# Optimization experiments

Measured on AMD Instinct MI355X. Metric: run time of the kernel, lower is better.

## Reference

```python
import jax, jax.numpy as jnp
import numpy as np

XI = 4.0  # init kwarg


def _gaussian_kernel(xi: float):
    radius = int(3 * xi)
    coords = jnp.arange(-radius, radius + 1, dtype=jnp.float32)
    g1 = jnp.exp(-coords ** 2 / (2 * xi * xi))
    g1 = g1 / g1.sum()
    # dense 3D outer-product kernel, shape (K, K, K)
    g3 = g1[:, None, None] * g1[None, :, None] * g1[None, None, :]
    K = g3.shape[0]
    # grouped depthwise weight: (out=3, in/groups=1, K, K, K)
    return jnp.broadcast_to(g3[None, None], (3, 1, K, K, K))


def setup_inputs() -> dict:
    key = jax.random.key(0)
    x = jax.random.normal(key, (1, 3, 160, 160, 160), dtype=jnp.float32)
    kernel = _gaussian_kernel(XI)
    return {"x": x, "kernel": kernel}


def reference(x, kernel):
    # grouped Conv3d, groups=3 (depthwise), 'same' padding of radius each side
    r = (kernel.shape[-1] - 1) // 2
    return jax.lax.conv_general_dilated(
        x, kernel,
        window_strides=(1, 1, 1),
        padding=[(r, r), (r, r), (r, r)],
        dimension_numbers=("NCDHW", "OIDHW", "NCDHW"),
        feature_group_count=3,
    )
```

## Files before the change

### kernel.cpp

```cpp
#include <hip/hip_runtime.h>
#include <hip/hip_fp16.h>


#define NV 160
constexpr int KS    = 25;
constexpr int RAD   = 12;
constexpr int PLANE = NV * NV;
constexpr int VOL   = NV * NV * NV;
constexpr int TOT   = 3 * VOL;
constexpr int ROWS  = NV + 2 * RAD;

constexpr int PITCH = 17;
constexpr int OPT   = 10;
constexpr int WIN   = OPT + KS - 1;
constexpr int OROW  = 168;

constexpr int HC2   = 80;
constexpr int TR    = HC2 + 2 * RAD;
constexpr int TP2   = 84;
constexpr int ATASK = 64 * 20;
constexpr int BTASK = 40 * 20;

__device__ __forceinline__ void pk(float2& a, float2 g, float2 v) {
    asm("v_pk_fma_f32 %0, %1, %2, %0" : "+v"(a) : "v"(g), "v"(v));
}

__device__ __forceinline__ void load_g(const float* __restrict__ k3, float* g) {
    float c   = k3[12 * 625 + 312];
    float g12 = cbrtf(c);
    float inv = 1.0f / (g12 * g12);
#pragma unroll
    for (int t = 0; t < KS; ++t) g[t] = k3[t * 625 + 312] * inv;
}

__global__ __launch_bounds__(256) void conv_w(const float* __restrict__ in,
                                              __half* __restrict__ out,
                                              const float* __restrict__ k3) {
    __shared__ float2 T[ROWS][PITCH];
    float gs[KS];
    load_g(k3, gs);
    float2 g2[KS];
#pragma unroll
    for (int t = 0; t < KS; ++t) g2[t] = make_float2(gs[t], gs[t]);

    int tid = threadIdx.x;
    int b   = blockIdx.x;
    int ht  = b % 5;
    int cd  = b / 5;
    int h0  = ht * 32;
    const float* base = in + (size_t)cd * PLANE;

    int wl = tid & 31, hq = tid >> 5;
#pragma unroll
    for (int hh = 0; hh < 2; ++hh) {
        int hp = hq + hh * 8;
        const float* r0 = base + (h0 + 2 * hp) * NV;
#pragma unroll
        for (int ib = 0; ib < ROWS; ib += 32) {
            int i = ib + wl;
            if (i < ROWS) {
                int wv = i - RAD;
                float a = 0.f, bb = 0.f;
                if (wv >= 0 && wv < NV) { a = r0[wv]; bb = r0[NV + wv]; }
                T[i][hp] = make_float2(a, bb);
            }
        }
    }
    __syncthreads();

    int p  = tid & 15;
    int ct = tid >> 4;
    int wb = ct * OPT;
    float2 acc[OPT];
#pragma unroll
    for (int j = 0; j < OPT; ++j) acc[j] = make_float2(0.f, 0.f);
#pragma unroll
    for (int it = 0; it < WIN; ++it) {
        float2 v = T[wb + it][p];
#pragma unroll
        for (int j = 0; j < OPT; ++j) {
            int t = it - j;
            if (t >= 0 && t < KS) pk(acc[j], g2[t], v);
        }
    }

    __syncthreads();
    __half* Ost = (__half*)(&T[0][0]);
#pragma unroll
    for (int j = 0; j < OPT; ++j) {
        Ost[(2 * p)     * OROW + wb + j] = __float2half_rn(acc[j].x);
        Ost[(2 * p + 1) * OROW + wb + j] = __float2half_rn(acc[j].y);
    }
    __syncthreads();
    __half* ob = out + (size_t)cd * PLANE + (size_t)h0 * NV;
#pragma unroll
    for (int it = 0; it < 3; ++it) {
        int task = it * 256 + tid;
        if (task < 640) {
            int chunk = task % 20, row = task / 20;
            uint4 v = *(const uint4*)(Ost + row * OROW + 8 * chunk);
            *(uint4*)(ob + (size_t)row * NV + 8 * chunk) = v;
        }
    }
}

__global__ __launch_bounds__(320) void conv_h(const __half* __restrict__ in,
                                              __half* __restrict__ out,
                                              const float* __restrict__ k3) {
    __shared__ __half2 T[TR][TP2];
    float gs[KS];
    load_g(k3, gs);
    float2 g2[KS];
#pragma unroll
    for (int t = 0; t < KS; ++t) g2[t] = make_float2(gs[t], gs[t]);

    int tid = threadIdx.x;
    int b   = blockIdx.x;
    int hh  = b & 1;
    int cd  = b >> 1;
    int h0  = hh * HC2;
    const __half* base = in + (size_t)cd * PLANE;

    uint4 rA[4];
#pragma unroll
    for (int i = 0; i < 4; ++i) {
        int task = i * 320 + tid;
        int r = task / 20, k = task % 20;
        int hg = h0 - RAD + r;
        rA[i] = make_uint4(0u, 0u, 0u, 0u);
        if (hg >= 0 && hg < NV) rA[i] = *(const uint4*)(base + hg * NV + 8 * k);
    }
#pragma unroll
    for (int i = 0; i < 4; ++i) {
        int task = i * 320 + tid;
        int r = task / 20, k = task % 20;
        *(uint4*)(&T[r][4 * k]) = rA[i];
    }
    uint4 rB[3];
#pragma unroll
    for (int i = 0; i < 3; ++i) {
        int task = i * 320 + tid;
        rB[i] = make_uint4(0u, 0u, 0u, 0u);
        if (task < BTASK) {
            int r = 64 + task / 20, k = task % 20;
            int hg = h0 - RAD + r;
            if (hg >= 0 && hg < NV) rB[i] = *(const uint4*)(base + hg * NV + 8 * k);
        }
    }
    asm volatile("s_waitcnt lgkmcnt(0)" ::: "memory");
    __builtin_amdgcn_s_barrier();
    __builtin_amdgcn_sched_barrier(0);

    int wp = tid % 80, oc = tid / 80;
    {
        int rb = oc * OPT;
        float2 acc[OPT];
#pragma unroll
        for (int j = 0; j < OPT; ++j) acc[j] = make_float2(0.f, 0.f);
#pragma unroll
        for (int it = 0; it < WIN; ++it) {
            float2 v = __half22float2(T[rb + it][wp]);
#pragma unroll
            for (int j = 0; j < OPT; ++j) {
                int t = it - j;
                if (t >= 0 && t < KS) pk(acc[j], g2[t], v);
            }
        }
        __half* op = out + (size_t)cd * PLANE + (size_t)(h0 + rb) * NV + 2 * wp;
#pragma unroll
        for (int j = 0; j < OPT; ++j)
            *(__half2*)(op + j * NV) = __float22half2_rn(acc[j]);
    }
    __builtin_amdgcn_sched_barrier(0);
#pragma unroll
    for (int i = 0; i < 3; ++i) {
        int task = i * 320 + tid;
        if (task < BTASK) {
            int r = 64 + task / 20, k = task % 20;
            *(uint4*)(&T[r][4 * k]) = rB[i];
        }
    }
    asm volatile("s_waitcnt lgkmcnt(0)" ::: "memory");
    __builtin_amdgcn_s_barrier();
    __builtin_amdgcn_sched_barrier(0);
    {
        int rb = (oc + 4) * OPT;
        float2 acc[OPT];
#pragma unroll
        for (int j = 0; j < OPT; ++j) acc[j] = make_float2(0.f, 0.f);
#pragma unroll
        for (int it = 0; it < WIN; ++it) {
            float2 v = __half22float2(T[rb + it][wp]);
#pragma unroll
            for (int j = 0; j < OPT; ++j) {
                int t = it - j;
                if (t >= 0 && t < KS) pk(acc[j], g2[t], v);
            }
        }
        __half* op = out + (size_t)cd * PLANE + (size_t)(h0 + rb) * NV + 2 * wp;
#pragma unroll
        for (int j = 0; j < OPT; ++j)
            *(__half2*)(op + j * NV) = __float22half2_rn(acc[j]);
    }
}

__global__ __launch_bounds__(320) void conv_d(const __half* __restrict__ in,
                                              float* __restrict__ out,
                                              const float* __restrict__ k3) {
    __shared__ __half2 T[TR][TP2];
    float gs[KS];
    load_g(k3, gs);
    float2 g2[KS];
#pragma unroll
    for (int t = 0; t < KS; ++t) g2[t] = make_float2(gs[t], gs[t]);

    int tid = threadIdx.x;
    int b   = blockIdx.x;
    int dh  = b & 1;
    int ch  = b >> 1;
    int c   = ch / NV, h = ch % NV;
    int d0  = dh * HC2;
    const __half* base = in + (size_t)c * VOL + h * NV;

    uint4 rA[4];
#pragma unroll
    for (int i = 0; i < 4; ++i) {
        int task = i * 320 + tid;
        int r = task / 20, k = task % 20;
        int dg = d0 - RAD + r;
        rA[i] = make_uint4(0u, 0u, 0u, 0u);
        if (dg >= 0 && dg < NV)
            rA[i] = *(const uint4*)(base + (size_t)dg * PLANE + 8 * k);
    }
#pragma unroll
    for (int i = 0; i < 4; ++i) {
        int task = i * 320 + tid;
        int r = task / 20, k = task % 20;
        *(uint4*)(&T[r][4 * k]) = rA[i];
    }
    uint4 rB[3];
#pragma unroll
    for (int i = 0; i < 3; ++i) {
        int task = i * 320 + tid;
        rB[i] = make_uint4(0u, 0u, 0u, 0u);
        if (task < BTASK) {
            int r = 64 + task / 20, k = task % 20;
            int dg = d0 - RAD + r;
            if (dg >= 0 && dg < NV)
                rB[i] = *(const uint4*)(base + (size_t)dg * PLANE + 8 * k);
        }
    }
    asm volatile("s_waitcnt lgkmcnt(0)" ::: "memory");
    __builtin_amdgcn_s_barrier();
    __builtin_amdgcn_sched_barrier(0);

    int wp = tid % 80, oc = tid / 80;
    {
        int rb = oc * OPT;
        float2 acc[OPT];
#pragma unroll
        for (int j = 0; j < OPT; ++j) acc[j] = make_float2(0.f, 0.f);
#pragma unroll
        for (int it = 0; it < WIN; ++it) {
            float2 v = __half22float2(T[rb + it][wp]);
#pragma unroll
            for (int j = 0; j < OPT; ++j) {
                int t = it - j;
                if (t >= 0 && t < KS) pk(acc[j], g2[t], v);
            }
        }
        float* op = out + (size_t)c * VOL + h * NV + 2 * wp;
#pragma unroll
        for (int j = 0; j < OPT; ++j)
            *(float2*)(op + (size_t)(d0 + rb + j) * PLANE) = acc[j];
    }
    __builtin_amdgcn_sched_barrier(0);
#pragma unroll
    for (int i = 0; i < 3; ++i) {
        int task = i * 320 + tid;
        if (task < BTASK) {
            int r = 64 + task / 20, k = task % 20;
            *(uint4*)(&T[r][4 * k]) = rB[i];
        }
    }
    asm volatile("s_waitcnt lgkmcnt(0)" ::: "memory");
    __builtin_amdgcn_s_barrier();
    __builtin_amdgcn_sched_barrier(0);
    {
        int rb = (oc + 4) * OPT;
        float2 acc[OPT];
#pragma unroll
        for (int j = 0; j < OPT; ++j) acc[j] = make_float2(0.f, 0.f);
#pragma unroll
        for (int it = 0; it < WIN; ++it) {
            float2 v = __half22float2(T[rb + it][wp]);
#pragma unroll
            for (int j = 0; j < OPT; ++j) {
                int t = it - j;
                if (t >= 0 && t < KS) pk(acc[j], g2[t], v);
            }
        }
        float* op = out + (size_t)c * VOL + h * NV + 2 * wp;
#pragma unroll
        for (int j = 0; j < OPT; ++j)
            *(float2*)(op + (size_t)(d0 + rb + j) * PLANE) = acc[j];
    }
}

__global__ __launch_bounds__(256) void conv3d_direct(const float* __restrict__ x,
                                                     const float* __restrict__ k3,
                                                     float* __restrict__ out) {
    int idx = blockIdx.x * 256 + threadIdx.x;
    if (idx >= TOT) return;
    int w = idx % NV;
    int t = idx / NV;
    int h = t % NV; t /= NV;
    int d = t % NV;
    int c = t / NV;
    const float* kc = k3 + c * (KS * KS * KS);
    float acc = 0.f;
    for (int i = 0; i < KS; ++i) {
        int dd = d + i - RAD;
        if (dd < 0 || dd >= NV) continue;
        for (int j = 0; j < KS; ++j) {
            int hh = h + j - RAD;
            if (hh < 0 || hh >= NV) continue;
            const float* xr = x + (c * NV + dd) * NV * NV + hh * NV + (w - RAD);
            const float* kr = kc + (i * KS + j) * KS;
            int k0 = (RAD - w) > 0 ? (RAD - w) : 0;
            int k1 = (NV + RAD - w) < KS ? (NV + RAD - w) : KS;
            for (int k = k0; k < k1; ++k) acc += kr[k] * xr[k];
        }
    }
    out[idx] = acc;
}

extern "C" void kernel_launch(void* const* d_in, const int* in_sizes, int n_in,
                              void* d_out, int out_size, void* d_ws, size_t ws_size,
                              hipStream_t stream) {
    const float* x  = (const float*)d_in[0];
    const float* k3 = (const float*)d_in[1];
    float* out = (float*)d_out;

    if (ws_size >= (size_t)TOT * 2 * sizeof(__half)) {
        __half* tmpA = (__half*)d_ws;
        __half* tmpB = tmpA + TOT;
        conv_w<<<2400, 256, 0, stream>>>(x, tmpA, k3);
        conv_h<<<480 * 2, 320, 0, stream>>>(tmpA, tmpB, k3);
        conv_d<<<480 * 2, 320, 0, stream>>>(tmpB, out, k3);
    } else {
        conv3d_direct<<<(TOT + 255) / 256, 256, 0, stream>>>(x, k3, out);
    }
}
```

Measured before the change: 61.28 us.

## Load conv_h/conv_d halo tiles directly into LDS with global_load_lds

Replaces the register-staged global-to-LDS copies in the H and D passes with direct global_load_lds DMA into an unpadded shared tile. Out-of-range halo rows are zero-filled by explicit LDS stores, and the tile base shifts per half. The second half of the tile is waited on with partial vmcnt counts, so the first compute pass overlaps the tail of the load. This removes register pressure and the VGPR round trip, but drops the padding that avoided bank conflicts and depends on exact vmcnt ordering for correctness.

```diff
diff --git a/kernel.cpp b/kernel.cpp
--- a/kernel.cpp
+++ b/kernel.cpp
@@ -15,11 +15,12 @@
 constexpr int WIN   = OPT + KS - 1;
 constexpr int OROW  = 168;
 
-constexpr int HC2   = 80;
-constexpr int TR    = HC2 + 2 * RAD;
-constexpr int TP2   = 84;
-constexpr int ATASK = 64 * 20;
-constexpr int BTASK = 40 * 20;
+constexpr int HC2    = 80;
+constexpr int TR     = 104;
+constexpr int TPW    = 80;
+constexpr int VROWS  = 92;
+constexpr int VSLOTS = VROWS * 20;
+constexpr int ZSLOTS = 12 * 20;
 
 __device__ __forceinline__ void pk(float2& a, float2 g, float2 v) {
     asm("v_pk_fma_f32 %0, %1, %2, %0" : "+v"(a) : "v"(g), "v"(v));
@@ -31,6 +32,12 @@
     float inv = 1.0f / (g12 * g12);
 #pragma unroll
     for (int t = 0; t < KS; ++t) g[t] = k3[t * 625 + 312] * inv;
+}
+
+__device__ __forceinline__ void gll16(const void* g, void* l) {
+    __builtin_amdgcn_global_load_lds(
+        (const __attribute__((address_space(1))) void*)g,
+        (__attribute__((address_space(3))) void*)l, 16, 0, 0);
 }
 
 __global__ __launch_bounds__(256) void conv_w(const float* __restrict__ in,
@@ -107,7 +114,7 @@
 __global__ __launch_bounds__(320) void conv_h(const __half* __restrict__ in,
                                               __half* __restrict__ out,
                                               const float* __restrict__ k3) {
-    __shared__ __half2 T[TR][TP2];
+    __shared__ __half2 T[TR][TPW];
     float gs[KS];
     load_g(k3, gs);
     float2 g2[KS];
@@ -119,35 +126,30 @@
     int hh  = b & 1;
     int cd  = b >> 1;
     int h0  = hh * HC2;
-    const __half* base = in + (size_t)cd * PLANE;
-
-    uint4 rA[4];
-#pragma unroll
-    for (int i = 0; i < 4; ++i) {
-        int task = i * 320 + tid;
-        int r = task / 20, k = task % 20;
-        int hg = h0 - RAD + r;
-        rA[i] = make_uint4(0u, 0u, 0u, 0u);
-        if (hg >= 0 && hg < NV) rA[i] = *(const uint4*)(base + hg * NV + 8 * k);
-    }
-#pragma unroll
-    for (int i = 0; i < 4; ++i) {
-        int task = i * 320 + tid;
-        int r = task / 20, k = task % 20;
-        *(uint4*)(&T[r][4 * k]) = rA[i];
-    }
-    uint4 rB[3];
-#pragma unroll
-    for (int i = 0; i < 3; ++i) {
-        int task = i * 320 + tid;
-        rB[i] = make_uint4(0u, 0u, 0u, 0u);
-        if (task < BTASK) {
-            int r = 64 + task / 20, k = task % 20;
-            int hg = h0 - RAD + r;
-            if (hg >= 0 && hg < NV) rB[i] = *(const uint4*)(base + hg * NV + 8 * k);
-        }
-    }
-    asm volatile("s_waitcnt lgkmcnt(0)" ::: "memory");
+    char* Tf = (char*)(&T[0][0]);
+
+    int zbase = (hh == 0) ? 0 : 92 * 320;
+    if (tid < ZSLOTS)
+        *(uint4*)(Tf + zbase + tid * 16) = make_uint4(0u, 0u, 0u, 0u);
+
+    int vbase = (hh == 0) ? 12 * 320 : 0;
+    const char* gsrc = (const char*)(in + (size_t)cd * PLANE
+                                     + (size_t)((hh == 0) ? 0 : 68) * NV);
+    int wavebase = tid & ~63;
+#pragma unroll
+    for (int it = 0; it < 4; ++it) {
+        int sw = it * 320 + wavebase;
+        gll16(gsrc + (size_t)(sw + (tid & 63)) * 16, Tf + vbase + sw * 16);
+    }
+#pragma unroll
+    for (int it = 4; it < 6; ++it) {
+        int slot = it * 320 + tid;
+        if (slot < VSLOTS) {
+            int sw = it * 320 + wavebase;
+            gll16(gsrc + (size_t)slot * 16, Tf + vbase + sw * 16);
+        }
+    }
+    asm volatile("s_waitcnt vmcnt(2) lgkmcnt(0)" ::: "memory");
     __builtin_amdgcn_s_barrier();
     __builtin_amdgcn_sched_barrier(0);
 
@@ -172,15 +174,7 @@
             *(__half2*)(op + j * NV) = __float22half2_rn(acc[j]);
     }
     __builtin_amdgcn_sched_barrier(0);
-#pragma unroll
-    for (int i = 0; i < 3; ++i) {
-        int task = i * 320 + tid;
-        if (task < BTASK) {
-            int r = 64 + task / 20, k = task % 20;
-            *(uint4*)(&T[r][4 * k]) = rB[i];
-        }
-    }
-    asm volatile("s_waitcnt lgkmcnt(0)" ::: "memory");
+    asm volatile("s_waitcnt vmcnt(0)" ::: "memory");
     __builtin_amdgcn_s_barrier();
     __builtin_amdgcn_sched_barrier(0);
     {
@@ -207,7 +201,7 @@
 __global__ __launch_bounds__(320) void conv_d(const __half* __restrict__ in,
                                               float* __restrict__ out,
                                               const float* __restrict__ k3) {
-    __shared__ __half2 T[TR][TP2];
+    __shared__ __half2 T[TR][TPW];
     float gs[KS];
     load_g(k3, gs);
     float2 g2[KS];
@@ -220,37 +214,34 @@
     int ch  = b >> 1;
     int c   = ch / NV, h = ch % NV;
     int d0  = dh * HC2;
-    const __half* base = in + (size_t)c * VOL + h * NV;
-
-    uint4 rA[4];
-#pragma unroll
-    for (int i = 0; i < 4; ++i) {
-        int task = i * 320 + tid;
-        int r = task / 20, k = task % 20;
-        int dg = d0 - RAD + r;
-        rA[i] = make_uint4(0u, 0u, 0u, 0u);
-        if (dg >= 0 && dg < NV)
-            rA[i] = *(const uint4*)(base + (size_t)dg * PLANE + 8 * k);
-    }
-#pragma unroll
-    for (int i = 0; i < 4; ++i) {
-        int task = i * 320 + tid;
-        int r = task / 20, k = task % 20;
-        *(uint4*)(&T[r][4 * k]) = rA[i];
-    }
-    uint4 rB[3];
-#pragma unroll
-    for (int i = 0; i < 3; ++i) {
-        int task = i * 320 + tid;
-        rB[i] = make_uint4(0u, 0u, 0u, 0u);
-        if (task < BTASK) {
-            int r = 64 + task / 20, k = task % 20;
-            int dg = d0 - RAD + r;
-            if (dg >= 0 && dg < NV)
-                rB[i] = *(const uint4*)(base + (size_t)dg * PLANE + 8 * k);
-        }
-    }
-    asm volatile("s_waitcnt lgkmcnt(0)" ::: "memory");
+    char* Tf = (char*)(&T[0][0]);
+
+    int zbase = (dh == 0) ? 0 : 92 * 320;
+    if (tid < ZSLOTS)
+        *(uint4*)(Tf + zbase + tid * 16) = make_uint4(0u, 0u, 0u, 0u);
+
+    int vbase = (dh == 0) ? 12 * 320 : 0;
+    int dg0   = (dh == 0) ? 0 : 68;
+    const char* gd = (const char*)(in + (size_t)c * VOL + h * NV
+                                   + (size_t)dg0 * PLANE);
+    int wavebase = tid & ~63;
+#pragma unroll
+    for (int it = 0; it < 4; ++it) {
+        int slot = it * 320 + tid;
+        int rr = slot / 20, cc = slot % 20;
+        int sw = it * 320 + wavebase;
+        gll16(gd + (size_t)rr * (PLANE * 2) + cc * 16, Tf + vbase + sw * 16);
+    }
+#pragma unroll
+    for (int it = 4; it < 6; ++it) {
+        int slot = it * 320 + tid;
+        if (slot < VSLOTS) {
+            int rr = slot / 20, cc = slot % 20;
+            int sw = it * 320 + wavebase;
+            gll16(gd + (size_t)rr * (PLANE * 2) + cc * 16, Tf + vbase + sw * 16);
+        }
+    }
+    asm volatile("s_waitcnt vmcnt(2) lgkmcnt(0)" ::: "memory");
     __builtin_amdgcn_s_barrier();
     __builtin_amdgcn_sched_barrier(0);
 
@@ -275,15 +266,7 @@
             *(float2*)(op + (size_t)(d0 + rb + j) * PLANE) = acc[j];
     }
     __builtin_amdgcn_sched_barrier(0);
-#pragma unroll
-    for (int i = 0; i < 3; ++i) {
-        int task = i * 320 + tid;
-        if (task < BTASK) {
-            int r = 64 + task / 20, k = task % 20;
-            *(uint4*)(&T[r][4 * k]) = rB[i];
-        }
-    }
-    asm volatile("s_waitcnt lgkmcnt(0)" ::: "memory");
+    asm volatile("s_waitcnt vmcnt(0)" ::: "memory");
     __builtin_amdgcn_s_barrier();
     __builtin_amdgcn_sched_barrier(0);
     {
```

Result: faster. 52.83 us (-13.8%).
